# Performance work log

Measured on AMD Instinct MI355X. Metric: run time of the kernel, lower is better.

## Reference

```python
import jax, jax.numpy as jnp
import numpy as np

N_NODES = 50000
N_EDGES = 600000
D = 128
L = 4
N_GRAPHS = 64
N_PATIENTS = 50
LAMBDA = 1.0

@jax.custom_vjp
def grl(x):
    return x

def _grl_fwd(x):
    return x, None

def _grl_bwd(_, g):
    return (-LAMBDA * g,)

grl.defvjp(_grl_fwd, _grl_bwd)


def setup_inputs() -> dict:
    key = jax.random.key(0)
    ks = jax.random.split(key, 16)
    x = jax.random.normal(ks[0], (N_NODES, D), dtype=jnp.float32)
    edge_index = jax.random.randint(ks[1], (2, N_EDGES), 0, N_NODES, dtype=jnp.int32)
    batch = jnp.sort(jax.random.randint(ks[2], (N_NODES,), 0, N_GRAPHS, dtype=jnp.int32))
    s = 1.0 / np.sqrt(D)
    W_root = jax.random.normal(ks[3], (L, D, D), dtype=jnp.float32) * s
    W_rel = jax.random.normal(ks[4], (L, D, D), dtype=jnp.float32) * s
    b_conv = jnp.zeros((L, D), dtype=jnp.float32)
    ln_gamma = jnp.ones((L, D), dtype=jnp.float32)
    ln_beta = jnp.zeros((L, D), dtype=jnp.float32)
    boundary_W = jax.random.normal(ks[5], (D, 1), dtype=jnp.float32) * s
    boundary_b = jnp.zeros((1,), dtype=jnp.float32)
    dom_W1 = jax.random.normal(ks[6], (D, D // 2), dtype=jnp.float32) * s
    dom_b1 = jnp.zeros((D // 2,), dtype=jnp.float32)
    dom_W2 = jax.random.normal(ks[7], (D // 2, N_PATIENTS), dtype=jnp.float32) * (1.0 / np.sqrt(D // 2))
    dom_b2 = jnp.zeros((N_PATIENTS,), dtype=jnp.float32)
    return {"x": x, "edge_index": edge_index, "batch": batch,
            "W_root": W_root, "W_rel": W_rel, "b_conv": b_conv,
            "ln_gamma": ln_gamma, "ln_beta": ln_beta,
            "boundary_W": boundary_W, "boundary_b": boundary_b,
            "dom_W1": dom_W1, "dom_b1": dom_b1,
            "dom_W2": dom_W2, "dom_b2": dom_b2}


def _layernorm(h, gamma, beta, eps=1e-5):
    mu = jnp.mean(h, axis=-1, keepdims=True)
    var = jnp.var(h, axis=-1, keepdims=True)
    return (h - mu) * jax.lax.rsqrt(var + eps) * gamma + beta


def reference(x, edge_index, batch, W_root, W_rel, b_conv, ln_gamma, ln_beta,
              boundary_W, boundary_b, dom_W1, dom_b1, dom_W2, dom_b2):
    src, dst = edge_index[0], edge_index[1]
    n = x.shape[0]
    for l in range(L):
        x_in = x
        msg = x[src] @ W_rel[l]                                   # [E, D] gather + GEMM
        agg = jax.ops.segment_sum(msg, dst, num_segments=n)        # [N, D] scatter-add
        h = x @ W_root[l] + agg + b_conv[l]
        h = _layernorm(h, ln_gamma[l], ln_beta[l])
        h = jax.nn.elu(h)
        # dropout p=model.dropout in eval mode -> identity
        x = h + x_in                                               # residual (shapes match)
    boundary_logits = (x @ boundary_W + boundary_b)[:, 0]          # [N]
    pooled = jax.ops.segment_sum(x, batch, num_segments=N_GRAPHS)  # [G, D]
    counts = jax.ops.segment_sum(jnp.ones((n, 1), x.dtype), batch, num_segments=N_GRAPHS)
    pooled = pooled / jnp.clip(counts, 1.0)
    r = grl(pooled)                                                # GRL: identity fwd
    h = jax.nn.elu(r @ dom_W1 + dom_b1)                            # Dropout(0.1) eval -> identity
    domain_logits = h @ dom_W2 + dom_b2                            # [G, n_patients]
    return boundary_logits, domain_logits
```

## Files before the change

kernel.cpp:

```cpp
#include <hip/hip_runtime.h>
#include <cstdint>
#include <cstddef>

#define N_NODES   50000
#define N_EDGES   600000
#define DIM       128
#define NLAYERS   4
#define N_GRAPHS  64
#define N_PATIENTS 50
#define ROWS      32

typedef __attribute__((ext_vector_type(8))) __bf16        bf16x8;
typedef __attribute__((ext_vector_type(4))) float         f32x4;
typedef __attribute__((ext_vector_type(4))) unsigned int  u32x4;
typedef __attribute__((ext_vector_type(8))) unsigned short u16x8;

__device__ inline unsigned short f2bf(float f) {
    unsigned u = __builtin_bit_cast(unsigned, f);
    u += 0x7FFFu + ((u >> 16) & 1u);
    return (unsigned short)(u >> 16);
}

__device__ inline float bf2f(unsigned short s) {
    return __builtin_bit_cast(float, (unsigned)s << 16);
}

__device__ inline f32x4 lo4(u16x8 u) {
    f32x4 r;
    r[0] = bf2f(u[0]); r[1] = bf2f(u[1]); r[2] = bf2f(u[2]); r[3] = bf2f(u[3]);
    return r;
}
__device__ inline f32x4 hi4(u16x8 u) {
    f32x4 r;
    r[0] = bf2f(u[4]); r[1] = bf2f(u[5]); r[2] = bf2f(u[6]); r[3] = bf2f(u[7]);
    return r;
}


__global__ void k_scan_a(const int* __restrict__ counts, int* __restrict__ incl,
                         int* __restrict__ bsums, int n) {
    __shared__ int s[256];
    int i = blockIdx.x * 256 + threadIdx.x;
    int v = (i < n) ? counts[i] : 0;
    s[threadIdx.x] = v;
    __syncthreads();
    for (int off = 1; off < 256; off <<= 1) {
        int t = (threadIdx.x >= off) ? s[threadIdx.x - off] : 0;
        __syncthreads();
        s[threadIdx.x] += t;
        __syncthreads();
    }
    if (i < n) incl[i] = s[threadIdx.x];
    if (threadIdx.x == 255) bsums[blockIdx.x] = s[255];
}

__global__ void k_scan_b(int* __restrict__ bsums, int nb) {
    __shared__ int s[256];
    int t = threadIdx.x;
    int v = (t < nb) ? bsums[t] : 0;
    s[t] = v;
    __syncthreads();
    for (int off = 1; off < 256; off <<= 1) {
        int u = (t >= off) ? s[t - off] : 0;
        __syncthreads();
        s[t] += u;
        __syncthreads();
    }
    if (t < nb) bsums[t] = s[t];
}

__global__ void k_scan_c(const int* __restrict__ counts, const int* __restrict__ incl,
                         const int* __restrict__ bsums, int* __restrict__ row_ptr,
                         int* __restrict__ cursor, int n) {
    int i = blockIdx.x * 256 + threadIdx.x;
    if (i < n) {
        int off = blockIdx.x ? bsums[blockIdx.x - 1] : 0;
        int ex  = incl[i] - counts[i] + off;
        row_ptr[i] = ex;
        cursor[i]  = ex;
        if (i == n - 1) row_ptr[n] = incl[i] + off;
    }
}

__global__ void k_fill(const int* __restrict__ ei, int* __restrict__ cursor,
                       int* __restrict__ esorted) {
    int e = blockIdx.x * 256 + threadIdx.x;
    if (e < N_EDGES) {
        int d   = ei[N_EDGES + e];
        int pos = atomicAdd(&cursor[d], 1);
        esorted[pos] = ei[e];
    }
}


__global__ void k_prep(const float* __restrict__ x, unsigned short* __restrict__ xb,
                       const float* __restrict__ Wroot, const float* __restrict__ Wrel,
                       unsigned short* __restrict__ Wt,
                       const int* __restrict__ ei, int* __restrict__ counts) {
    int idx = blockIdx.x * 256 + threadIdx.x;
    if (idx < N_NODES * DIM / 8) {
        f32x4 v0 = *(const f32x4*)(x + (size_t)idx * 8);
        f32x4 v1 = *(const f32x4*)(x + (size_t)idx * 8 + 4);
        u16x8 o = { f2bf(v0[0]), f2bf(v0[1]), f2bf(v0[2]), f2bf(v0[3]),
                    f2bf(v1[0]), f2bf(v1[1]), f2bf(v1[2]), f2bf(v1[3]) };
        *(u16x8*)(xb + (size_t)idx * 8) = o;
    }
    if (idx < NLAYERS * DIM * 256) {
        int l = idx >> 15;
        int c = (idx >> 8) & 127;
        int k = idx & 255;
        float v = (k < 128) ? Wroot[l * 16384 + k * 128 + c]
                            : Wrel[l * 16384 + (k - 128) * 128 + c];
        Wt[idx] = f2bf(v);
    }
    if (idx < N_EDGES) atomicAdd(&counts[ei[N_EDGES + idx]], 1);
}


__global__ __launch_bounds__(512, 8) void k_layer(
    const float* __restrict__ xin,
    const unsigned short* __restrict__ xb,
    float* __restrict__ xout,
    unsigned short* __restrict__ xbnext,
    const int* __restrict__ row_ptr, const int* __restrict__ esrc,
    const unsigned short* __restrict__ Wt,
    const float* __restrict__ bconv, const float* __restrict__ gamma,
    const float* __restrict__ beta,
    const float* __restrict__ bW, const float* __restrict__ bb,
    float* __restrict__ boundary, int last)
{
    __shared__ __align__(16) unsigned short x2s[ROWS * 256];
    __shared__ __align__(16) float xf[ROWS * 132];
    __shared__ float rsum[ROWS][4], rsq[ROWS][4], rbl[ROWS][4];
    const int tid     = threadIdx.x;
    const int rowbase = blockIdx.x * ROWS;
    const int lane = tid & 63, w = tid >> 6;

    const int grp = tid >> 4;
    const int li  = tid & 15;

    {
        int grow = rowbase + grp;
        int rx = (grp & 7) << 4;
        u16x8 v = { 0, 0, 0, 0, 0, 0, 0, 0 };
        f32x4 f0 = 0.f, f1 = 0.f;
        if (grow < N_NODES) {
            v  = *(const u16x8*)(xb + (size_t)grow * DIM + li * 8);
            f0 = *(const f32x4*)(xin + (size_t)grow * DIM + li * 8);
            f1 = *(const f32x4*)(xin + (size_t)grow * DIM + li * 8 + 4);
        }
        int byteoff = (grp * 512 + li * 16) ^ rx;
        *(u16x8*)((char*)x2s + byteoff) = v;
        *(f32x4*)(&xf[grp * 132 + li * 8])     = f0;
        *(f32x4*)(&xf[grp * 132 + li * 8 + 4]) = f1;
    }

    {
        int grow = rowbase + grp;
        f32x4 a0 = 0.f, a1 = 0.f, b0 = 0.f, b1 = 0.f;
        int beg = 0, end = 0;
        if (grow < N_NODES) { beg = row_ptr[grow]; end = row_ptr[grow + 1]; }
        int e = beg;
        for (; e + 5 < end; e += 6) {
            int s0 = esrc[e],     s1 = esrc[e + 1], s2 = esrc[e + 2];
            int s3 = esrc[e + 3], s4 = esrc[e + 4], s5 = esrc[e + 5];
            u16x8 u0 = *(const u16x8*)(xb + (size_t)s0 * DIM + li * 8);
            u16x8 u1 = *(const u16x8*)(xb + (size_t)s1 * DIM + li * 8);
            u16x8 u2 = *(const u16x8*)(xb + (size_t)s2 * DIM + li * 8);
            u16x8 u3 = *(const u16x8*)(xb + (size_t)s3 * DIM + li * 8);
            u16x8 u4 = *(const u16x8*)(xb + (size_t)s4 * DIM + li * 8);
            u16x8 u5 = *(const u16x8*)(xb + (size_t)s5 * DIM + li * 8);
            a0 += lo4(u0); a1 += hi4(u0);
            b0 += lo4(u1); b1 += hi4(u1);
            a0 += lo4(u2); a1 += hi4(u2);
            b0 += lo4(u3); b1 += hi4(u3);
            a0 += lo4(u4); a1 += hi4(u4);
            b0 += lo4(u5); b1 += hi4(u5);
        }
        for (; e < end; ++e) {
            int s0 = esrc[e];
            u16x8 u0 = *(const u16x8*)(xb + (size_t)s0 * DIM + li * 8);
            a0 += lo4(u0); a1 += hi4(u0);
        }
        a0 += b0; a1 += b1;
        u16x8 o = { f2bf(a0[0]), f2bf(a0[1]), f2bf(a0[2]), f2bf(a0[3]),
                    f2bf(a1[0]), f2bf(a1[1]), f2bf(a1[2]), f2bf(a1[3]) };
        int byteoff = (grp * 512 + 256 + li * 16) ^ ((grp & 7) << 4);
        *(u16x8*)((char*)x2s + byteoff) = o;
    }
    __syncthreads();

    int colb = lane & 15, kg = lane >> 4;
    int rt = w >> 2, cq = w & 3;

    u32x4 araw[8];
    {
        int row  = rt * 16 + colb;
        int base = row * 512 + kg * 16;
        int rx   = (row & 7) << 4;
        #pragma unroll
        for (int ks = 0; ks < 8; ks++) {
            int byteoff = (base + ks * 64) ^ rx;
            araw[ks] = *(const u32x4*)((const char*)x2s + byteoff);
        }
    }

    f32x4 acc[2];
    acc[0] = 0.0f; acc[1] = 0.0f;

    #pragma unroll
    for (int cb = 0; cb < 2; cb++) {
        const unsigned short* wp = Wt + ((cq * 32 + cb * 16 + colb) * 256 + kg * 8);
        #pragma unroll
        for (int ks = 0; ks < 8; ks++) {
            u32x4 braw = *(const u32x4*)(wp + ks * 32);
            acc[cb] = __builtin_amdgcn_mfma_f32_16x16x32_bf16(
                __builtin_bit_cast(bf16x8, araw[ks]),
                __builtin_bit_cast(bf16x8, braw), acc[cb], 0, 0, 0);
        }
    }

    float hv[4][2];
    #pragma unroll
    for (int j = 0; j < 4; j++) {
        float ps = 0.f, pq = 0.f;
        #pragma unroll
        for (int cb = 0; cb < 2; cb++) {
            int col = cq * 32 + cb * 16 + colb;
            float h = acc[cb][j] + bconv[col];
            hv[j][cb] = h; ps += h; pq += h * h;
        }
        #pragma unroll
        for (int m = 1; m < 16; m <<= 1) {
            ps += __shfl_xor(ps, m);
            pq += __shfl_xor(pq, m);
        }
        if (colb == 0) {
            int lr = rt * 16 + kg * 4 + j;
            rsum[lr][cq] = ps;
            rsq[lr][cq]  = pq;
        }
    }
    __syncthreads();

    #pragma unroll
    for (int j = 0; j < 4; j++) {
        int lr   = rt * 16 + kg * 4 + j;
        int grow = rowbase + lr;
        float sum = rsum[lr][0] + rsum[lr][1] + rsum[lr][2] + rsum[lr][3];
        float sq  = rsq[lr][0] + rsq[lr][1] + rsq[lr][2] + rsq[lr][3];
        float mean = sum * (1.f / 128.f);
        float var  = sq * (1.f / 128.f) - mean * mean;
        float rs   = rsqrtf(var + 1e-5f);
        float bl = 0.f;
        if (grow < N_NODES) {
            #pragma unroll
            for (int cb = 0; cb < 2; cb++) {
                int col  = cq * 32 + cb * 16 + colb;
                float hn = (hv[j][cb] - mean) * rs * gamma[col] + beta[col];
                hn = hn > 0.f ? hn : (expf(hn) - 1.f);
                float xo = hn + xf[lr * 132 + col];
                xout[(size_t)grow * DIM + col] = xo;
                if (xbnext) xbnext[(size_t)grow * DIM + col] = f2bf(xo);
                bl += xo * bW[col];
            }
        }
        if (last) {
            #pragma unroll
            for (int m = 1; m < 16; m <<= 1) bl += __shfl_xor(bl, m);
            if (colb == 0) rbl[lr][cq] = bl;
        }
    }
    if (last) {
        __syncthreads();
        if (tid < ROWS && rowbase + tid < N_NODES)
            boundary[rowbase + tid] = rbl[tid][0] + rbl[tid][1] + rbl[tid][2] + rbl[tid][3] + bb[0];
    }
}


__global__ void k_pool(const float* __restrict__ x, const int* __restrict__ batch,
                       float* __restrict__ pooled, int* __restrict__ gcount) {
    __shared__ float s[128];
    int g = blockIdx.x >> 4, q = blockIdx.x & 15;
    int lo = 0, hi = N_NODES;
    while (lo < hi) { int m = (lo + hi) >> 1; if (batch[m] < g) lo = m + 1; else hi = m; }
    int s0 = lo;
    lo = 0; hi = N_NODES;
    while (lo < hi) { int m = (lo + hi) >> 1; if (batch[m] < g + 1) lo = m + 1; else hi = m; }
    int e0  = lo;
    int len = e0 - s0;
    int r0 = s0 + (int)((long long)len * q / 16);
    int r1 = s0 + (int)((long long)len * (q + 1) / 16);
    int col = threadIdx.x & 127, half = threadIdx.x >> 7;
    float acc = 0.f;
    for (int r = r0 + half; r < r1; r += 2) acc += x[(size_t)r * DIM + col];
    if (half) s[col] = acc;
    __syncthreads();
    if (!half) {
        acc += s[col];
        atomicAdd(&pooled[g * DIM + col], acc);
    }
    if (q == 0 && threadIdx.x == 0) gcount[g] = len;
}


__global__ __launch_bounds__(256) void k_dom1(
    const float* __restrict__ pooled, const int* __restrict__ gcount,
    const float* __restrict__ W1, const float* __restrict__ b1,
    float* __restrict__ h1g)
{
    int o = blockIdx.x * 256 + threadIdx.x;
    if (o < 64 * 64) {
        int i = o >> 6, j = o & 63;
        float cnt = (float)gcount[i];
        float rc = 1.f / (cnt < 1.f ? 1.f : cnt);
        float s = b1[j];
        #pragma unroll 8
        for (int k = 0; k < 128; k++) s += pooled[i * 128 + k] * rc * W1[k * 64 + j];
        h1g[o] = s > 0.f ? s : (expf(s) - 1.f);
    }
}

__global__ __launch_bounds__(256) void k_dom2(
    const float* __restrict__ h1g,
    const float* __restrict__ W2, const float* __restrict__ b2,
    float* __restrict__ out)
{
    int o = blockIdx.x * 256 + threadIdx.x;
    if (o < 64 * N_PATIENTS) {
        int i = o / N_PATIENTS, p = o - i * N_PATIENTS;
        float s = b2[p];
        #pragma unroll 8
        for (int k = 0; k < 64; k++) s += h1g[i * 64 + k] * W2[k * N_PATIENTS + p];
        out[o] = s;
    }
}


extern "C" void kernel_launch(void* const* d_in, const int* in_sizes, int n_in,
                              void* d_out, int out_size, void* d_ws, size_t ws_size,
                              hipStream_t stream) {
    const float* x     = (const float*)d_in[0];
    const int*   ei    = (const int*)d_in[1];
    const int*   batch = (const int*)d_in[2];
    const float* Wroot = (const float*)d_in[3];
    const float* Wrel  = (const float*)d_in[4];
    const float* bconv = (const float*)d_in[5];
    const float* gamma = (const float*)d_in[6];
    const float* beta  = (const float*)d_in[7];
    const float* bW    = (const float*)d_in[8];
    const float* bb    = (const float*)d_in[9];
    const float* W1    = (const float*)d_in[10];
    const float* b1    = (const float*)d_in[11];
    const float* W2    = (const float*)d_in[12];
    const float* b2    = (const float*)d_in[13];
    float* out = (float*)d_out;

    char* ws = (char*)d_ws;
    size_t off = 0;
    auto alloc = [&](size_t bytes) -> char* {
        char* p = ws + off;
        off += (bytes + 255) & ~(size_t)255;
        return p;
    };
    float*          xA      = (float*)alloc((size_t)N_NODES * DIM * 4);
    float*          xB      = (float*)alloc((size_t)N_NODES * DIM * 4);
    unsigned short* xbA     = (unsigned short*)alloc((size_t)N_NODES * DIM * 2);
    unsigned short* xbB     = (unsigned short*)alloc((size_t)N_NODES * DIM * 2);
    unsigned short* Wt      = (unsigned short*)alloc((size_t)NLAYERS * DIM * 256 * 2);
    int*            counts  = (int*)alloc((size_t)N_NODES * 4);
    int*            incl    = (int*)alloc((size_t)N_NODES * 4);
    int*            row_ptr = (int*)alloc((size_t)(N_NODES + 1) * 4);
    int*            cursor  = (int*)alloc((size_t)N_NODES * 4);
    int*            esorted = (int*)alloc((size_t)N_EDGES * 4);
    int*            bsums   = (int*)alloc(256 * 4);
    float*          pooled  = (float*)alloc((size_t)N_GRAPHS * DIM * 4);
    int*            gcount  = (int*)alloc((size_t)N_GRAPHS * 4);
    float*          h1g     = (float*)alloc((size_t)64 * 64 * 4);
    (void)ws_size; (void)in_sizes; (void)n_in; (void)out_size;

    hipMemsetAsync(counts, 0, (size_t)N_NODES * 4, stream);
    hipMemsetAsync(pooled, 0, (size_t)N_GRAPHS * DIM * 4, stream);

    k_prep<<<(N_NODES * DIM / 8 + 255) / 256, 256, 0, stream>>>(x, xbA, Wroot, Wrel, Wt, ei, counts);
    int nb = (N_NODES + 255) / 256;
    k_scan_a<<<nb, 256, 0, stream>>>(counts, incl, bsums, N_NODES);
    k_scan_b<<<1, 256, 0, stream>>>(bsums, nb);
    k_scan_c<<<nb, 256, 0, stream>>>(counts, incl, bsums, row_ptr, cursor, N_NODES);
    k_fill<<<(N_EDGES + 255) / 256, 256, 0, stream>>>(ei, cursor, esorted);

    int lgrid = (N_NODES + ROWS - 1) / ROWS;
    const float* xi = x;
    float* xo = xA;
    const unsigned short* xbi = xbA;
    unsigned short* xbo = xbB;
    for (int l = 0; l < NLAYERS; l++) {
        int last = (l == NLAYERS - 1);
        k_layer<<<lgrid, 512, 0, stream>>>(xi, xbi, xo, last ? nullptr : xbo,
                                           row_ptr, esorted, Wt + (size_t)l * DIM * 256,
                                           bconv + l * DIM, gamma + l * DIM, beta + l * DIM,
                                           bW, bb, out, last);
        xi = xo;
        xo = (xo == xA) ? xB : xA;
        const unsigned short* t = xbi; xbi = xbo; xbo = (unsigned short*)t;
    }
    k_pool<<<N_GRAPHS * 16, 256, 0, stream>>>(xi, batch, pooled, gcount);
    k_dom1<<<16, 256, 0, stream>>>(pooled, gcount, W1, b1, h1g);
    k_dom2<<<(64 * N_PATIENTS + 255) / 256, 256, 0, stream>>>(h1g, W2, b2, out + N_NODES);
}
```

Measured before the change: 345.4 us.

## Make layer kernel persistent with warp-specialized gather/MFMA double-buffered pipeline

Turns k_layer into a persistent kernel over 512 blocks. Six warps gather neighbour sums and stage the next tile into double-buffered shared memory while two warps run MFMA, LayerNorm and the epilogue on the previous tile. The residual input is now kept in shared memory as a bf16 hi/lo pair, which cuts shared memory use, and each MFMA warp covers all 128 columns so row statistics need no cross-warp reduction. The aim is to overlap the latency-bound gather with compute. The cost is fewer compute warps, a lower occupancy hint and per-tile barriers that tie the two warp roles together.

```diff
diff --git a/kernel.cpp b/kernel.cpp
--- a/kernel.cpp
+++ b/kernel.cpp
@@ -9,6 +9,8 @@
 #define N_GRAPHS  64
 #define N_PATIENTS 50
 #define ROWS      32
+#define NT_TILES  1563
+#define GRIDL     512
 
 typedef __attribute__((ext_vector_type(8))) __bf16        bf16x8;
 typedef __attribute__((ext_vector_type(4))) float         f32x4;
@@ -117,7 +119,7 @@
 }
 
 
-__global__ __launch_bounds__(512, 8) void k_layer(
+__global__ __launch_bounds__(512, 4) void k_layer(
     const float* __restrict__ xin,
     const unsigned short* __restrict__ xb,
     float* __restrict__ xout,
@@ -129,152 +131,146 @@
     const float* __restrict__ bW, const float* __restrict__ bb,
     float* __restrict__ boundary, int last)
 {
-    __shared__ __align__(16) unsigned short x2s[ROWS * 256];
-    __shared__ __align__(16) float xf[ROWS * 132];
-    __shared__ float rsum[ROWS][4], rsq[ROWS][4], rbl[ROWS][4];
-    const int tid     = threadIdx.x;
-    const int rowbase = blockIdx.x * ROWS;
+    __shared__ __align__(16) unsigned short x2s[2][ROWS * 256];
+    __shared__ __align__(16) unsigned short los[2][ROWS * 136];
+    const int tid  = threadIdx.x;
     const int lane = tid & 63, w = tid >> 6;
-
-    const int grp = tid >> 4;
-    const int li  = tid & 15;
-
-    {
-        int grow = rowbase + grp;
-        int rx = (grp & 7) << 4;
-        u16x8 v = { 0, 0, 0, 0, 0, 0, 0, 0 };
-        f32x4 f0 = 0.f, f1 = 0.f;
-        if (grow < N_NODES) {
-            v  = *(const u16x8*)(xb + (size_t)grow * DIM + li * 8);
-            f0 = *(const f32x4*)(xin + (size_t)grow * DIM + li * 8);
-            f1 = *(const f32x4*)(xin + (size_t)grow * DIM + li * 8 + 4);
-        }
-        int byteoff = (grp * 512 + li * 16) ^ rx;
-        *(u16x8*)((char*)x2s + byteoff) = v;
-        *(f32x4*)(&xf[grp * 132 + li * 8])     = f0;
-        *(f32x4*)(&xf[grp * 132 + li * 8 + 4]) = f1;
-    }
-
-    {
-        int grow = rowbase + grp;
-        f32x4 a0 = 0.f, a1 = 0.f, b0 = 0.f, b1 = 0.f;
-        int beg = 0, end = 0;
-        if (grow < N_NODES) { beg = row_ptr[grow]; end = row_ptr[grow + 1]; }
-        int e = beg;
-        for (; e + 5 < end; e += 6) {
-            int s0 = esrc[e],     s1 = esrc[e + 1], s2 = esrc[e + 2];
-            int s3 = esrc[e + 3], s4 = esrc[e + 4], s5 = esrc[e + 5];
-            u16x8 u0 = *(const u16x8*)(xb + (size_t)s0 * DIM + li * 8);
-            u16x8 u1 = *(const u16x8*)(xb + (size_t)s1 * DIM + li * 8);
-            u16x8 u2 = *(const u16x8*)(xb + (size_t)s2 * DIM + li * 8);
-            u16x8 u3 = *(const u16x8*)(xb + (size_t)s3 * DIM + li * 8);
-            u16x8 u4 = *(const u16x8*)(xb + (size_t)s4 * DIM + li * 8);
-            u16x8 u5 = *(const u16x8*)(xb + (size_t)s5 * DIM + li * 8);
-            a0 += lo4(u0); a1 += hi4(u0);
-            b0 += lo4(u1); b1 += hi4(u1);
-            a0 += lo4(u2); a1 += hi4(u2);
-            b0 += lo4(u3); b1 += hi4(u3);
-            a0 += lo4(u4); a1 += hi4(u4);
-            b0 += lo4(u5); b1 += hi4(u5);
-        }
-        for (; e < end; ++e) {
-            int s0 = esrc[e];
-            u16x8 u0 = *(const u16x8*)(xb + (size_t)s0 * DIM + li * 8);
-            a0 += lo4(u0); a1 += hi4(u0);
-        }
-        a0 += b0; a1 += b1;
-        u16x8 o = { f2bf(a0[0]), f2bf(a0[1]), f2bf(a0[2]), f2bf(a0[3]),
-                    f2bf(a1[0]), f2bf(a1[1]), f2bf(a1[2]), f2bf(a1[3]) };
-        int byteoff = (grp * 512 + 256 + li * 16) ^ ((grp & 7) << 4);
-        *(u16x8*)((char*)x2s + byteoff) = o;
-    }
-    __syncthreads();
-
-    int colb = lane & 15, kg = lane >> 4;
-    int rt = w >> 2, cq = w & 3;
-
-    u32x4 araw[8];
-    {
-        int row  = rt * 16 + colb;
-        int base = row * 512 + kg * 16;
-        int rx   = (row & 7) << 4;
-        #pragma unroll
-        for (int ks = 0; ks < 8; ks++) {
-            int byteoff = (base + ks * 64) ^ rx;
-            araw[ks] = *(const u32x4*)((const char*)x2s + byteoff);
-        }
-    }
-
-    f32x4 acc[2];
-    acc[0] = 0.0f; acc[1] = 0.0f;
-
-    #pragma unroll
-    for (int cb = 0; cb < 2; cb++) {
-        const unsigned short* wp = Wt + ((cq * 32 + cb * 16 + colb) * 256 + kg * 8);
-        #pragma unroll
-        for (int ks = 0; ks < 8; ks++) {
-            u32x4 braw = *(const u32x4*)(wp + ks * 32);
-            acc[cb] = __builtin_amdgcn_mfma_f32_16x16x32_bf16(
-                __builtin_bit_cast(bf16x8, araw[ks]),
-                __builtin_bit_cast(bf16x8, braw), acc[cb], 0, 0, 0);
-        }
-    }
-
-    float hv[4][2];
-    #pragma unroll
-    for (int j = 0; j < 4; j++) {
-        float ps = 0.f, pq = 0.f;
-        #pragma unroll
-        for (int cb = 0; cb < 2; cb++) {
-            int col = cq * 32 + cb * 16 + colb;
-            float h = acc[cb][j] + bconv[col];
-            hv[j][cb] = h; ps += h; pq += h * h;
-        }
-        #pragma unroll
-        for (int m = 1; m < 16; m <<= 1) {
-            ps += __shfl_xor(ps, m);
-            pq += __shfl_xor(pq, m);
-        }
-        if (colb == 0) {
-            int lr = rt * 16 + kg * 4 + j;
-            rsum[lr][cq] = ps;
-            rsq[lr][cq]  = pq;
-        }
-    }
-    __syncthreads();
-
-    #pragma unroll
-    for (int j = 0; j < 4; j++) {
-        int lr   = rt * 16 + kg * 4 + j;
-        int grow = rowbase + lr;
-        float sum = rsum[lr][0] + rsum[lr][1] + rsum[lr][2] + rsum[lr][3];
-        float sq  = rsq[lr][0] + rsq[lr][1] + rsq[lr][2] + rsq[lr][3];
-        float mean = sum * (1.f / 128.f);
-        float var  = sq * (1.f / 128.f) - mean * mean;
-        float rs   = rsqrtf(var + 1e-5f);
-        float bl = 0.f;
-        if (grow < N_NODES) {
+    const int nt = 3 + (blockIdx.x < (NT_TILES - 3 * GRIDL) ? 1 : 0);
+
+    for (int p = 0; p <= nt; ++p) {
+        if (w >= 2 && p < nt) {
+            int tile = blockIdx.x + p * GRIDL;
+            int rowbase = tile * ROWS;
+            unsigned short* xs = x2s[p & 1];
+            unsigned short* ls = los[p & 1];
+            int group = (w - 2) * 4 + (lane >> 4);
+            int li = lane & 15;
             #pragma unroll
-            for (int cb = 0; cb < 2; cb++) {
-                int col  = cq * 32 + cb * 16 + colb;
-                float hn = (hv[j][cb] - mean) * rs * gamma[col] + beta[col];
-                hn = hn > 0.f ? hn : (expf(hn) - 1.f);
-                float xo = hn + xf[lr * 132 + col];
-                xout[(size_t)grow * DIM + col] = xo;
-                if (xbnext) xbnext[(size_t)grow * DIM + col] = f2bf(xo);
-                bl += xo * bW[col];
+            for (int rr = 0; rr < 2; ++rr) {
+                int row = (rr == 0) ? group : (group < 8 ? 24 + group : -1);
+                if (row < 0) break;
+                int grow = rowbase + row;
+                int rx = (row & 7) << 4;
+                u16x8 h = { 0, 0, 0, 0, 0, 0, 0, 0 };
+                u16x8 l = { 0, 0, 0, 0, 0, 0, 0, 0 };
+                if (grow < N_NODES) {
+                    f32x4 f0 = *(const f32x4*)(xin + (size_t)grow * DIM + li * 8);
+                    f32x4 f1 = *(const f32x4*)(xin + (size_t)grow * DIM + li * 8 + 4);
+                    #pragma unroll
+                    for (int j = 0; j < 4; j++) {
+                        unsigned short hh = f2bf(f0[j]);
+                        h[j] = hh; l[j] = f2bf(f0[j] - bf2f(hh));
+                    }
+                    #pragma unroll
+                    for (int j = 0; j < 4; j++) {
+                        unsigned short hh = f2bf(f1[j]);
+                        h[4 + j] = hh; l[4 + j] = f2bf(f1[j] - bf2f(hh));
+                    }
+                }
+                *(u16x8*)((char*)xs + ((row * 512 + li * 16) ^ rx)) = h;
+                *(u16x8*)(ls + row * 136 + li * 8) = l;
+                f32x4 a0 = 0.f, a1 = 0.f, b0 = 0.f, b1 = 0.f;
+                int beg = 0, end = 0;
+                if (grow < N_NODES) { beg = row_ptr[grow]; end = row_ptr[grow + 1]; }
+                int e = beg;
+                for (; e + 5 < end; e += 6) {
+                    int s0 = esrc[e],     s1 = esrc[e + 1], s2 = esrc[e + 2];
+                    int s3 = esrc[e + 3], s4 = esrc[e + 4], s5 = esrc[e + 5];
+                    u16x8 u0 = *(const u16x8*)(xb + (size_t)s0 * DIM + li * 8);
+                    u16x8 u1 = *(const u16x8*)(xb + (size_t)s1 * DIM + li * 8);
+                    u16x8 u2 = *(const u16x8*)(xb + (size_t)s2 * DIM + li * 8);
+                    u16x8 u3 = *(const u16x8*)(xb + (size_t)s3 * DIM + li * 8);
+                    u16x8 u4 = *(const u16x8*)(xb + (size_t)s4 * DIM + li * 8);
+                    u16x8 u5 = *(const u16x8*)(xb + (size_t)s5 * DIM + li * 8);
+                    a0 += lo4(u0); a1 += hi4(u0);
+                    b0 += lo4(u1); b1 += hi4(u1);
+                    a0 += lo4(u2); a1 += hi4(u2);
+                    b0 += lo4(u3); b1 += hi4(u3);
+                    a0 += lo4(u4); a1 += hi4(u4);
+                    b0 += lo4(u5); b1 += hi4(u5);
+                }
+                for (; e < end; ++e) {
+                    int s0 = esrc[e];
+                    u16x8 u0 = *(const u16x8*)(xb + (size_t)s0 * DIM + li * 8);
+                    a0 += lo4(u0); a1 += hi4(u0);
+                }
+                a0 += b0; a1 += b1;
+                u16x8 o = { f2bf(a0[0]), f2bf(a0[1]), f2bf(a0[2]), f2bf(a0[3]),
+                            f2bf(a1[0]), f2bf(a1[1]), f2bf(a1[2]), f2bf(a1[3]) };
+                *(u16x8*)((char*)xs + ((row * 512 + 256 + li * 16) ^ rx)) = o;
             }
         }
-        if (last) {
+
+        if (w < 2 && p > 0) {
+            int tile = blockIdx.x + (p - 1) * GRIDL;
+            int rowbase = tile * ROWS;
+            const unsigned short* xs = x2s[(p - 1) & 1];
+            const unsigned short* ls = los[(p - 1) & 1];
+            int colb = lane & 15, kg = lane >> 4;
+            int arow  = w * 16 + colb;
+            int abase = arow * 512 + kg * 16;
+            int arx   = (arow & 7) << 4;
+
+            f32x4 acc[8];
             #pragma unroll
-            for (int m = 1; m < 16; m <<= 1) bl += __shfl_xor(bl, m);
-            if (colb == 0) rbl[lr][cq] = bl;
+            for (int cb = 0; cb < 8; cb++) acc[cb] = 0.0f;
+
+            #pragma unroll
+            for (int ks = 0; ks < 8; ks++) {
+                u32x4 a = *(const u32x4*)((const char*)xs + ((abase + ks * 64) ^ arx));
+                #pragma unroll
+                for (int cb = 0; cb < 8; cb++) {
+                    u32x4 braw = *(const u32x4*)(Wt + ((cb * 16 + colb) * 256 + kg * 8) + ks * 32);
+                    acc[cb] = __builtin_amdgcn_mfma_f32_16x16x32_bf16(
+                        __builtin_bit_cast(bf16x8, a),
+                        __builtin_bit_cast(bf16x8, braw), acc[cb], 0, 0, 0);
+                }
+            }
+
+            #pragma unroll
+            for (int j = 0; j < 4; j++) {
+                int lr   = w * 16 + kg * 4 + j;
+                int grow = rowbase + lr;
+                float hv[8];
+                float ps = 0.f, pq = 0.f;
+                #pragma unroll
+                for (int cb = 0; cb < 8; cb++) {
+                    float h = acc[cb][j] + bconv[cb * 16 + colb];
+                    hv[cb] = h; ps += h; pq += h * h;
+                }
+                #pragma unroll
+                for (int m = 1; m < 16; m <<= 1) {
+                    ps += __shfl_xor(ps, m);
+                    pq += __shfl_xor(pq, m);
+                }
+                float mean = ps * (1.f / 128.f);
+                float var  = pq * (1.f / 128.f) - mean * mean;
+                float rs   = rsqrtf(var + 1e-5f);
+                float bl = 0.f;
+                if (grow < N_NODES) {
+                    int rx = (lr & 7) << 4;
+                    #pragma unroll
+                    for (int cb = 0; cb < 8; cb++) {
+                        int col  = cb * 16 + colb;
+                        float hn = (hv[cb] - mean) * rs * gamma[col] + beta[col];
+                        hn = hn > 0.f ? hn : (expf(hn) - 1.f);
+                        int hoff = (lr * 512 + col * 2) ^ rx;
+                        float xi = bf2f(*(const unsigned short*)((const char*)xs + hoff))
+                                 + bf2f(ls[lr * 136 + col]);
+                        float xo = hn + xi;
+                        xout[(size_t)grow * DIM + col] = xo;
+                        if (xbnext) xbnext[(size_t)grow * DIM + col] = f2bf(xo);
+                        bl += xo * bW[col];
+                    }
+                }
+                if (last) {
+                    #pragma unroll
+                    for (int m = 1; m < 16; m <<= 1) bl += __shfl_xor(bl, m);
+                    if (colb == 0 && grow < N_NODES) boundary[grow] = bl + bb[0];
+                }
+            }
         }
-    }
-    if (last) {
         __syncthreads();
-        if (tid < ROWS && rowbase + tid < N_NODES)
-            boundary[rowbase + tid] = rbl[tid][0] + rbl[tid][1] + rbl[tid][2] + rbl[tid][3] + bb[0];
     }
 }
 
@@ -390,14 +386,13 @@
     k_scan_c<<<nb, 256, 0, stream>>>(counts, incl, bsums, row_ptr, cursor, N_NODES);
     k_fill<<<(N_EDGES + 255) / 256, 256, 0, stream>>>(ei, cursor, esorted);
 
-    int lgrid = (N_NODES + ROWS - 1) / ROWS;
     const float* xi = x;
     float* xo = xA;
     const unsigned short* xbi = xbA;
     unsigned short* xbo = xbB;
     for (int l = 0; l < NLAYERS; l++) {
         int last = (l == NLAYERS - 1);
-        k_layer<<<lgrid, 512, 0, stream>>>(xi, xbi, xo, last ? nullptr : xbo,
+        k_layer<<<GRIDL, 512, 0, stream>>>(xi, xbi, xo, last ? nullptr : xbo,
                                            row_ptr, esorted, Wt + (size_t)l * DIM * 256,
                                            bconv + l * DIM, gamma + l * DIM, beta + l * DIM,
                                            bW, bb, out, last);
```

New measurement: 802.1 us. +132.3%, slower.
